# Kernel tuning notes

Measured on AMD Instinct MI355X. Metric: run time of the kernel, lower is better.

The kernel has to match this reference:

```python
import jax, jax.numpy as jnp
import numpy as np

H1, H2, F1, F2 = 16, 16, 8, 1

def gcn_conv(x, src, dst, W, b, n_nodes):
    # PyG GCNConv: add self-loops (done by caller), deg-normalized mean-style aggregation
    h = x @ W  # [N, out]
    deg = jax.ops.segment_sum(jnp.ones_like(dst, dtype=h.dtype), dst, num_segments=n_nodes)
    dinv = jnp.where(deg > 0, deg ** -0.5, 0.0)
    norm = dinv[src] * dinv[dst]  # [E]
    agg = jax.ops.segment_sum(h[src] * norm[:, None], dst, num_segments=n_nodes)
    return agg + b


def setup_inputs() -> dict:
    key = jax.random.key(0)
    ks = jax.random.split(key, 12)
    N, E, G, NG = 320000, 5120000, 1000, 32
    x = jax.random.normal(ks[0], (N, 1), dtype=jnp.float32)
    edge_index = jax.random.randint(ks[1], (2, E), 0, N, dtype=jnp.int64)
    y = jax.random.normal(ks[2], (NG * G,), dtype=jnp.float32)
    gene_idx = jax.random.randint(ks[3], (1, G), 0, N // NG, dtype=jnp.int64)
    s = lambda fi, fo: (2.0 / (fi + fo)) ** 0.5
    return {
        'x': x, 'edge_index': edge_index, 'y': y, 'gene_idx': gene_idx, 'num_graphs': NG,
        'W1': jax.random.normal(ks[4], (1, H1), dtype=jnp.float32) * s(1, H1),
        'b1': jnp.zeros((H1,), dtype=jnp.float32),
        'W2': jax.random.normal(ks[5], (H1, H2), dtype=jnp.float32) * s(H1, H2),
        'b2': jnp.zeros((H2,), dtype=jnp.float32),
        'fc1_W': jax.random.normal(ks[6], (H2, F1), dtype=jnp.float32) * s(H2, F1),
        'fc1_b': jnp.zeros((F1,), dtype=jnp.float32),
        'fc2_W': jax.random.normal(ks[7], (F1, F2), dtype=jnp.float32) * s(F1, F2),
        'fc2_b': jnp.zeros((F2,), dtype=jnp.float32),
    }


def reference(x, edge_index, y, gene_idx, num_graphs, W1, b1, W2, b2, fc1_W, fc1_b, fc2_W, fc2_b):
    N = x.shape[0]
    loops = jnp.arange(N, dtype=edge_index.dtype)
    src = jnp.concatenate([edge_index[0], loops])
    dst = jnp.concatenate([edge_index[1], loops])

    h = jax.nn.relu(gcn_conv(x, src, dst, W1, b1, N))
    # F.dropout(p=0.4) is a no-op for a deterministic reference (identity at eval)
    h = jax.nn.relu(gcn_conv(h, src, dst, W2, b2, N))

    # vectorized form of the python gather loop: idx + i * nodes_per_graph, i = 0..reps-1
    nodes_per_graph = N // num_graphs
    reps = y.shape[0] // gene_idx.shape[1]
    offsets = (jnp.arange(reps, dtype=gene_idx.dtype) * nodes_per_graph)[:, None]
    all_idx = (gene_idx[0][None, :] + offsets).reshape(-1)  # [reps*G]
    t = h[all_idx]  # [reps*G, 16]

    t = jax.nn.relu(t @ fc1_W + fc1_b)
    return t @ fc2_W + fc2_b
```

## Files before the change

kernel.cpp:

```cpp
#include <hip/hip_runtime.h>


#define MAXB 17
#define RS_BITS 10
#define RS (1 << RS_BITS)
#define SRC_BITS 19
#define SRC_MASK ((1u << SRC_BITS) - 1u)
#define SENT 0xFFFFFFFFu
#define CMAX 160
#define NPGW_MAX 2048
#define HB 512
#define BK_BT 512
#define BK_EPT 16
#define BK_TILE (BK_BT * BK_EPT)
#define PAD4(x) (((x) + 3) & ~3)

__device__ __forceinline__ int div_npg(int d, unsigned long long magic) {
    return (int)(((unsigned long long)(unsigned)d * magic) >> 45);
}

__global__ void k_fill_f(float* __restrict__ w, float v, int n) {
    int i = blockIdx.x * blockDim.x + threadIdx.x;
    if (i < n) w[i] = v;
}
__global__ void k_fill_i(int* __restrict__ w, int v, int n) {
    int i = blockIdx.x * blockDim.x + threadIdx.x;
    if (i < n) w[i] = v;
}

__global__ void k_gprep(const float* __restrict__ W1, const float* __restrict__ b1,
                        const int* __restrict__ gene_idx,
                        float* __restrict__ bnd, int* __restrict__ prepI,
                        int* __restrict__ gmap, unsigned* __restrict__ gbit,
                        int* __restrict__ histT, int* __restrict__ histM,
                        int G, int npg, int npgw, int R) {
    int t = threadIdx.x;
    for (int i = t; i < npg; i += 256) gmap[i] = -1;
    for (int i = t; i < npgw; i += 256) gbit[i] = 0;
    for (int i = t; i < R; i += 256) { histT[i] = 0; histM[i] = 0; }
    __syncthreads();
    for (int g = t; g < G; g += 256) {
        int gi = gene_idx[g];
        if ((unsigned)gi < (unsigned)npg) {
            gmap[gi] = g;
            atomicOr(&gbit[gi >> 5], 1u << (gi & 31));
        }
    }
    if (t != 0) return;
    float tt[16]; int type[16]; int pos[16];
    float thr[16]; int nt = 0;
    for (int j = 0; j < 16; j++) {
        float W = W1[j], B = b1[j];
        if (W > 0.f)      { type[j] = 0; tt[j] = -B / W; }
        else if (W < 0.f) { type[j] = 1; tt[j] = -B / W; }
        else              { type[j] = (B > 0.f) ? 2 : 3; tt[j] = 0.f; }
    }
    for (int j = 0; j < 16; j++) {
        if (type[j] > 1) continue;
        float v = tt[j];
        int k = 0; while (k < nt && thr[k] < v) k++;
        if (!(k < nt && thr[k] == v)) {
            for (int m = nt; m > k; m--) thr[m] = thr[m - 1];
            thr[k] = v; nt++;
        }
    }
    int K = nt + 1;
    for (int j = 0; j < 16; j++) {
        if (type[j] <= 1) { int k = 0; while (thr[k] != tt[j]) k++; pos[j] = k; }
        else pos[j] = 0;
    }
    for (int k = 0; k < 16; k++) bnd[k] = (k < nt) ? thr[k] : 3.4e38f;
    prepI[0] = K;
    for (int k = 0; k < K; k++) {
        unsigned m = 0;
        for (int j = 0; j < 16; j++) {
            bool act;
            if (type[j] == 0)      act = (k >= pos[j] + 1);
            else if (type[j] == 1) act = (k <= pos[j]);
            else                   act = (type[j] == 2);
            if (act) m |= (1u << j);
        }
        prepI[1 + k] = (int)m;
    }
}

__global__ void k_cmap_hist(const int* __restrict__ gmap, const unsigned* __restrict__ gbit,
                            const int* __restrict__ dst,
                            int* __restrict__ cm, int* __restrict__ cslot, int* __restrict__ mc,
                            int* __restrict__ histT, int* __restrict__ histM,
                            int N, int R, int npg, int reps, int G, int E, int npgw,
                            unsigned long long magic) {
    __shared__ unsigned bitL[NPGW_MAX];
    for (int i = threadIdx.x; i < npgw; i += 256) bitL[i] = gbit[i];
    if (blockIdx.x < (unsigned)R) {
        __shared__ int cnt;
        if (threadIdx.x == 0) cnt = 0;
        __syncthreads();
        int r = blockIdx.x;
        int b0 = r << RS_BITS;
        for (int i = threadIdx.x; i < RS; i += 256) {
            int v = b0 + i;
            if (v >= N) continue;
            int rep = div_npg(v, magic);
            int gi = v - rep * npg;
            int out = -1;
            if (rep < reps && ((bitL[gi >> 5] >> (gi & 31)) & 1u)) {
                int g = gmap[gi];
                if (g >= 0) {
                    int sl = rep * G + g;
                    int c = atomicAdd(&cnt, 1);
                    if (c < CMAX) { cslot[r * CMAX + c] = sl; out = c; }
                    else out = -(sl + 2);
                }
            }
            cm[v] = out;
        }
        __syncthreads();
        if (threadIdx.x == 0) mc[r] = min(cnt, CMAX);
    } else {
        __shared__ int hT[512], hM[512];
        for (int i = threadIdx.x; i < R; i += 256) { hT[i] = 0; hM[i] = 0; }
        __syncthreads();
        int hb = blockIdx.x - R;
        int stride = HB * 256;
        int E4 = E >> 2;
        const int4* d4p = (const int4*)dst;
        for (int e = hb * 256 + threadIdx.x; e < E4; e += stride) {
            int4 d4 = d4p[e];
            int dd[4] = {d4.x, d4.y, d4.z, d4.w};
#pragma unroll
            for (int k = 0; k < 4; k++) {
                int d = dd[k];
                if ((unsigned)d >= (unsigned)N) continue;
                atomicAdd(&hT[d >> RS_BITS], 1);
                int rep = div_npg(d, magic);
                int gi = d - rep * npg;
                if (rep < reps && ((bitL[gi >> 5] >> (gi & 31)) & 1u))
                    atomicAdd(&hM[d >> RS_BITS], 1);
            }
        }
        for (int e = (E4 << 2) + hb * 256 + threadIdx.x; e < E; e += stride) {
            int d = dst[e];
            if ((unsigned)d >= (unsigned)N) continue;
            atomicAdd(&hT[d >> RS_BITS], 1);
            int rep = div_npg(d, magic);
            int gi = d - rep * npg;
            if (rep < reps && ((bitL[gi >> 5] >> (gi & 31)) & 1u))
                atomicAdd(&hM[d >> RS_BITS], 1);
        }
        __syncthreads();
        for (int i = threadIdx.x; i < R; i += 256) {
            if (hT[i]) atomicAdd(&histT[i], hT[i]);
            if (hM[i]) atomicAdd(&histM[i], hM[i]);
        }
    }
}

__global__ void k_scan(const int* __restrict__ histT, const int* __restrict__ histM,
                       int* __restrict__ baseA, unsigned long long* __restrict__ cur64,
                       unsigned* __restrict__ bucket, int R, int cap) {
    __shared__ int a[512];
    int t = threadIdx.x;
    int m = (t < R) ? histM[t] : 0;
    int tot = (t < R) ? histT[t] : 0;
    int u = tot - m; if (u < 0) u = 0;
    int seg = PAD4(m) + PAD4(u);
    a[t] = seg;
    __syncthreads();
    for (int off = 1; off < 512; off <<= 1) {
        int add = (t >= off) ? a[t - off] : 0;
        __syncthreads();
        a[t] += add;
        __syncthreads();
    }
    if (t < R) {
        int base = a[t] - seg;
        baseA[t] = base;
        int mstart = base, ustart = base + PAD4(m);
        cur64[t] = (unsigned long long)(unsigned)mstart |
                   ((unsigned long long)(unsigned)ustart << 32);
        for (int i = m; i < PAD4(m); i++) { int ix = mstart + i; if (ix < cap) bucket[ix] = SENT; }
        for (int i = u; i < PAD4(u); i++) { int ix = ustart + i; if (ix < cap) bucket[ix] = SENT; }
    }
}

__global__ void __launch_bounds__(BK_BT)
k_bucket(const int* __restrict__ src, const int* __restrict__ dst,
         const unsigned* __restrict__ gbit, unsigned long long* __restrict__ cur64,
         unsigned* __restrict__ bucket, int E, int N, int R, int cap,
         int npg, int reps, int npgw, unsigned long long magic) {
    __shared__ unsigned bitL[NPGW_MAX];
    __shared__ int cntA[512], cntB[512], mb[512], ub[512];
    for (int i = threadIdx.x; i < npgw; i += BK_BT) bitL[i] = gbit[i];
    for (int i = threadIdx.x; i < R; i += BK_BT) { cntA[i] = 0; cntB[i] = 0; }
    __syncthreads();
    int tile0 = blockIdx.x * BK_TILE;
    int rr[BK_EPT]; unsigned val[BK_EPT]; unsigned mbits = 0;
#pragma unroll
    for (int c = 0; c < 4; c++) {
        int e0 = tile0 + c * (BK_BT * 4) + threadIdx.x * 4;
        int dd[4], ss[4];
        if (e0 + 3 < E) {
            int4 d4 = *(const int4*)(dst + e0);
            int4 s4 = *(const int4*)(src + e0);
            dd[0] = d4.x; dd[1] = d4.y; dd[2] = d4.z; dd[3] = d4.w;
            ss[0] = s4.x; ss[1] = s4.y; ss[2] = s4.z; ss[3] = s4.w;
        } else {
#pragma unroll
            for (int k = 0; k < 4; k++) {
                int e = e0 + k;
                dd[k] = (e < E) ? dst[e] : -1;
                ss[k] = (e < E) ? src[e] : -1;
            }
        }
#pragma unroll
        for (int k = 0; k < 4; k++) {
            int idx = c * 4 + k;
            int d = dd[k];
            rr[idx] = -1;
            if ((unsigned)d < (unsigned)N) {
                int rep = div_npg(d, magic);
                int gi = d - rep * npg;
                unsigned m = (rep < reps && ((bitL[gi >> 5] >> (gi & 31)) & 1u)) ? 1u : 0u;
                int s = ss[k];
                rr[idx] = d >> RS_BITS;
                val[idx] = ((unsigned)s < (unsigned)N)
                               ? (((unsigned)(d & (RS - 1)) << SRC_BITS) | (unsigned)s)
                               : SENT;
                mbits |= m << idx;
                atomicAdd(&cntA[d >> RS_BITS], m ? 1 : (1 << 16));
            }
        }
    }
    __syncthreads();
    for (int r = threadIdx.x; r < R; r += BK_BT) {
        int c = cntA[r];
        if (c) {
            unsigned long long add = (unsigned long long)(c & 0xFFFF) |
                                     ((unsigned long long)(unsigned)(c >> 16) << 32);
            unsigned long long old = atomicAdd(&cur64[r], add);
            mb[r] = (int)(old & 0xFFFFFFFFull);
            ub[r] = (int)(old >> 32);
        }
    }
    __syncthreads();
#pragma unroll
    for (int i = 0; i < BK_EPT; i++) {
        int r = rr[i];
        if (r < 0) continue;
        unsigned m = (mbits >> i) & 1u;
        int o = atomicAdd(&cntB[r], m ? 1 : (1 << 16));
        int idx = m ? (mb[r] + (o & 0xFFFF)) : (ub[r] + (o >> 16));
        if ((unsigned)idx < (unsigned)cap) bucket[idx] = val[i];
    }
}


__global__ void __launch_bounds__(1024)
k_degR2(const unsigned* __restrict__ bucket, const int* __restrict__ baseA,
        const int* __restrict__ histT, const int* __restrict__ histM,
        int* __restrict__ pDeg, int cap, int S) {
    __shared__ int degL[RS];
    int r = blockIdx.x / S, q = blockIdx.x % S;
    int m = histM[r];
    int u = histT[r] - m; if (u < 0) u = 0;
    int nb = baseA[r];
    int len = min(PAD4(m) + PAD4(u), cap - nb);
    if (len < 0) len = 0;
    int lo = (int)(((long long)len * q / S) & ~3LL);
    int hi = (q == S - 1) ? len : (int)(((long long)len * (q + 1) / S) & ~3LL);
    for (int i = threadIdx.x; i < RS; i += blockDim.x) degL[i] = 0;
    __syncthreads();
    for (int i = lo + threadIdx.x * 4; i < hi; i += blockDim.x * 4) {
        uint4 e4 = *(const uint4*)(bucket + nb + i);
        if (i + 0 < hi && e4.x != SENT) atomicAdd(&degL[e4.x >> SRC_BITS], 1);
        if (i + 1 < hi && e4.y != SENT) atomicAdd(&degL[e4.y >> SRC_BITS], 1);
        if (i + 2 < hi && e4.z != SENT) atomicAdd(&degL[e4.z >> SRC_BITS], 1);
        if (i + 3 < hi && e4.w != SENT) atomicAdd(&degL[e4.w >> SRC_BITS], 1);
    }
    __syncthreads();
    int* out = pDeg + (size_t)(r * S + q) * RS;
    for (int i = threadIdx.x; i < RS; i += blockDim.x) out[i] = degL[i];
}

__global__ void k_dinvp2(const int* __restrict__ pDeg, const float* __restrict__ x,
                         float* __restrict__ sd, float* __restrict__ p, int N, int S) {
    int v = blockIdx.x * blockDim.x + threadIdx.x;
    if (v >= N) return;
    int r = v >> RS_BITS, l = v & (RS - 1);
    int deg = 0;
    for (int q = 0; q < S; q++) deg += pDeg[(size_t)(r * S + q) * RS + l];
    float di = rsqrtf((float)deg + 1.0f);
    sd[2 * v + 1] = di;
    p[v] = x[v] * di;
}

__global__ void __launch_bounds__(1024)
k_t1R2(const unsigned* __restrict__ bucket, const int* __restrict__ baseA,
       const int* __restrict__ histT, const int* __restrict__ histM,
       const float* __restrict__ p, float* __restrict__ pT1, int cap, int S) {
    __shared__ float accL[RS];
    int r = blockIdx.x / S, q = blockIdx.x % S;
    int m = histM[r];
    int u = histT[r] - m; if (u < 0) u = 0;
    int nb = baseA[r];
    int len = min(PAD4(m) + PAD4(u), cap - nb);
    if (len < 0) len = 0;
    int lo = (int)(((long long)len * q / S) & ~3LL);
    int hi = (q == S - 1) ? len : (int)(((long long)len * (q + 1) / S) & ~3LL);
    for (int i = threadIdx.x; i < RS; i += blockDim.x) accL[i] = 0.f;
    __syncthreads();
    for (int i = lo + threadIdx.x * 4; i < hi; i += blockDim.x * 4) {
        uint4 e4 = *(const uint4*)(bucket + nb + i);
        if (i + 0 < hi && e4.x != SENT) atomicAdd(&accL[e4.x >> SRC_BITS], p[e4.x & SRC_MASK]);
        if (i + 1 < hi && e4.y != SENT) atomicAdd(&accL[e4.y >> SRC_BITS], p[e4.y & SRC_MASK]);
        if (i + 2 < hi && e4.z != SENT) atomicAdd(&accL[e4.z >> SRC_BITS], p[e4.z & SRC_MASK]);
        if (i + 3 < hi && e4.w != SENT) atomicAdd(&accL[e4.w >> SRC_BITS], p[e4.w & SRC_MASK]);
    }
    __syncthreads();
    float* out = pT1 + (size_t)(r * S + q) * RS;
    for (int i = threadIdx.x; i < RS; i += blockDim.x) out[i] = accL[i];
}

__global__ void k_s3(const float* __restrict__ pT1, const float* __restrict__ p,
                     float* __restrict__ sd, float* __restrict__ aggb8, int n8,
                     int N, int S) {
    int v = blockIdx.x * blockDim.x + threadIdx.x;
    if (v < n8) aggb8[v] = 0.f;
    if (v >= N) return;
    int r = v >> RS_BITS, l = v & (RS - 1);
    float t1 = 0.f;
    for (int q = 0; q < S; q++) t1 += pT1[(size_t)(r * S + q) * RS + l];
    sd[2 * v] = sd[2 * v + 1] * (t1 + p[v]);
}

__global__ void k_aggS(const unsigned* __restrict__ bucket, const int* __restrict__ baseA,
                       const int* __restrict__ histM,
                       const float* __restrict__ sd, const int* __restrict__ cm,
                       const int* __restrict__ cslot, const int* __restrict__ mc,
                       const float* __restrict__ bnd, const int* __restrict__ prepI,
                       float* __restrict__ aggb8, int N, int cap) {
    __shared__ float acc[CMAX * 8];
    __shared__ int cmapL[RS];
    __shared__ float sB[3];
    __shared__ int sK;
    if (threadIdx.x == 0) sK = prepI[0];
    if (threadIdx.x < 3) sB[threadIdx.x] = bnd[threadIdx.x];
    __syncthreads();
    int K = sK;
    if (K > 4) return;
    int r = blockIdx.x;
    int b0 = r << RS_BITS;
    for (int i = threadIdx.x; i < RS; i += 256) {
        int v = b0 + i;
        cmapL[i] = (v < N) ? cm[v] : -1;
    }
    for (int i = threadIdx.x; i < CMAX * 8; i += 256) acc[i] = 0.f;
    __syncthreads();
    int nb = baseA[r];
    int mlen = min(histM[r], cap - nb);
    if (mlen < 0) mlen = 0;
    const float2* sd2 = (const float2*)sd;
    for (int i = threadIdx.x * 4; i < mlen; i += 256 * 4) {
        uint4 e4 = *(const uint4*)(bucket + nb + i);
        unsigned ee[4] = {e4.x, e4.y, e4.z, e4.w};
#pragma unroll
        for (int k4 = 0; k4 < 4; k4++) {
            if (i + k4 >= mlen) break;
            unsigned e = ee[k4];
            if (e == SENT) continue;
            int c = cmapL[e >> SRC_BITS];
            if (c == -1) continue;
            float2 v = sd2[e & SRC_MASK];
            int b = 0;
            for (int k = 0; k < K - 1; k++) b += (v.x > sB[k]) ? 1 : 0;
            if (c >= 0) {
                atomicAdd(&acc[c * 8 + 2 * b], v.x * v.y);
                atomicAdd(&acc[c * 8 + 2 * b + 1], v.y);
            } else {
                int sl = -(c + 2);
                atomicAdd(&aggb8[(size_t)sl * 8 + 2 * b], v.x * v.y);
                atomicAdd(&aggb8[(size_t)sl * 8 + 2 * b + 1], v.y);
            }
        }
    }
    __syncthreads();
    int mcR = mc[r];
    for (int idx = threadIdx.x; idx < mcR * 8; idx += 256) {
        int c = idx >> 3, j = idx & 7;
        int sl = cslot[r * CMAX + c];
        if (sl >= 0) aggb8[(size_t)sl * 8 + j] = acc[idx];
    }
}

__global__ void k_fillWide(const int* __restrict__ prepI, float* __restrict__ wide, int n) {
    if (prepI[0] <= 4) return;
    for (int i = blockIdx.x * blockDim.x + threadIdx.x; i < n; i += gridDim.x * blockDim.x)
        wide[i] = 0.f;
}


__global__ void k_mark(const int* __restrict__ gene_idx, int* __restrict__ slot,
                       int G, int M, int npg, int N) {
    int i = blockIdx.x * blockDim.x + threadIdx.x;
    if (i >= M) return;
    int node = gene_idx[i % G] + (i / G) * npg;
    if ((unsigned)node < (unsigned)N) slot[node] = i;
}

__global__ void k_deg(const int* __restrict__ dst, float* __restrict__ deg, int E, int N) {
    int e = blockIdx.x * blockDim.x + threadIdx.x;
    if (e >= E) return;
    int d = dst[e];
    if ((unsigned)d < (unsigned)N) atomicAdd(&deg[d], 1.0f);
}

__global__ void k_dinv_p(const float* __restrict__ x, float* __restrict__ degv,
                         float* __restrict__ p, int N) {
    int v = blockIdx.x * blockDim.x + threadIdx.x;
    if (v < N) {
        float di = rsqrtf(degv[v] + 1.0f);
        degv[v] = di;
        p[v] = x[v] * di;
    }
}

__global__ void k_scatter1(const int* __restrict__ src, const int* __restrict__ dst,
                           const float* __restrict__ p, float* __restrict__ t1, int E, int N) {
    int e = blockIdx.x * blockDim.x + threadIdx.x;
    if (e >= E) return;
    int s = src[e];
    int d = dst[e];
    if ((unsigned)s < (unsigned)N && (unsigned)d < (unsigned)N)
        atomicAdd(&t1[d], p[s]);
}

__global__ void k_s(const float* __restrict__ p, const float* __restrict__ dinv,
                    float* __restrict__ t1, int N) {
    int v = blockIdx.x * blockDim.x + threadIdx.x;
    if (v < N) t1[v] = dinv[v] * (t1[v] + p[v]);
}

__global__ void k_agg_atomic(const int* __restrict__ src, const int* __restrict__ dst,
                             const float* __restrict__ sA, const float* __restrict__ dA,
                             int str, const int* __restrict__ cm, const int* __restrict__ cslot,
                             const float* __restrict__ bnd, const int* __restrict__ prepI,
                             float* __restrict__ wide, int E, int N, int force, int mode) {
    __shared__ float sB[16];
    __shared__ int sK;
    if (threadIdx.x == 0) sK = prepI[0];
    if (threadIdx.x < 16) sB[threadIdx.x] = bnd[threadIdx.x];
    __syncthreads();
    int K = sK;
    if (!force && K <= 4) return;
    int T = K - 1;
    for (int e = blockIdx.x * blockDim.x + threadIdx.x; e < E; e += gridDim.x * blockDim.x) {
        int d = dst[e];
        if ((unsigned)d >= (unsigned)N) continue;
        int c = cm[d];
        int sl;
        if (mode == 0) sl = c;
        else sl = (c >= 0) ? cslot[(d >> RS_BITS) * CMAX + c] : (c <= -2 ? -(c + 2) : -1);
        if (sl < 0) continue;
        int sv = src[e];
        if ((unsigned)sv >= (unsigned)N) continue;
        float sval = sA[(size_t)sv * str];
        float di = dA[(size_t)sv * str];
        int b = 0;
        for (int i = 0; i < T; i++) b += (sval > sB[i]) ? 1 : 0;
        float* row = wide + (size_t)sl * (2 * MAXB) + 2 * b;
        atomicAdd(row, sval * di);
        atomicAdd(row + 1, di);
    }
}

__global__ void k_final(const float* __restrict__ aggb8, const float* __restrict__ wide,
                        const float* __restrict__ sA, const float* __restrict__ dA, int str,
                        const int* __restrict__ gene_idx, const int* __restrict__ cm,
                        const int* __restrict__ cslot, const int* __restrict__ prepI,
                        const float* __restrict__ W1, const float* __restrict__ b1,
                        const float* __restrict__ W2, const float* __restrict__ b2,
                        const float* __restrict__ f1W, const float* __restrict__ f1b,
                        const float* __restrict__ f2W, const float* __restrict__ f2b,
                        float* __restrict__ out, int G, int M, int npg, int N, int mode) {
    __shared__ float sW1[16], sb1[16], sW2[256], sb2[16], sf1[128], sf1b[8], sf2[8], sf2b[1];
    __shared__ int sMask[MAXB], sK;
    for (int i = threadIdx.x; i < 256; i += blockDim.x) sW2[i] = W2[i];
    for (int i = threadIdx.x; i < 128; i += blockDim.x) sf1[i] = f1W[i];
    if (threadIdx.x < 16) { sW1[threadIdx.x] = W1[threadIdx.x]; sb1[threadIdx.x] = b1[threadIdx.x]; sb2[threadIdx.x] = b2[threadIdx.x]; }
    if (threadIdx.x < 8)  { sf1b[threadIdx.x] = f1b[threadIdx.x]; sf2[threadIdx.x] = f2W[threadIdx.x]; }
    if (threadIdx.x == 0) { sf2b[0] = f2b[0]; sK = prepI[0]; }
    if (threadIdx.x < MAXB) sMask[threadIdx.x] = prepI[1 + threadIdx.x];
    __syncthreads();

    int i = blockIdx.x * blockDim.x + threadIdx.x;
    if (i >= M) return;
    int node = gene_idx[i % G] + (i / G) * npg;
    if ((unsigned)node >= (unsigned)N) { out[i] = 0.0f; return; }
    int K = sK;
    int c = cm[node];
    int sl;
    if (mode == 0) sl = c;
    else sl = (c >= 0) ? cslot[(node >> RS_BITS) * CMAX + c] : (c <= -2 ? -(c + 2) : -1);

    float di = dA[(size_t)node * str];
    float sval = sA[(size_t)node * str];

    float bu[MAXB], bw[MAXB];
    if (sl >= 0) {
        const float* row = (mode == 1 && K <= 4) ? (aggb8 + (size_t)sl * 8)
                                                 : (wide + (size_t)sl * (2 * MAXB));
        for (int k = 0; k < K; k++) { bu[k] = row[2 * k]; bw[k] = row[2 * k + 1]; }
    } else {
        for (int k = 0; k < K; k++) { bu[k] = 0.f; bw[k] = 0.f; }
    }

    float a[16];
#pragma unroll
    for (int j = 0; j < 16; j++) {
        float Su = 0.f, Sw = 0.f;
        for (int k = 0; k < K; k++) {
            if ((sMask[k] >> j) & 1) { Su += bu[k]; Sw += bw[k]; }
        }
        float aggj = sW1[j] * Su + sb1[j] * Sw;
        float qself = fmaxf(fmaf(sW1[j], sval, sb1[j]), 0.0f) * di;
        a[j] = di * (aggj + qself);
    }
    float h2[16];
#pragma unroll
    for (int j = 0; j < 16; j++) {
        float acc = sb2[j];
#pragma unroll
        for (int k = 0; k < 16; k++) acc = fmaf(a[k], sW2[k * 16 + j], acc);
        h2[j] = fmaxf(acc, 0.0f);
    }
    float f1[8];
#pragma unroll
    for (int j = 0; j < 8; j++) {
        float acc = sf1b[j];
#pragma unroll
        for (int k = 0; k < 16; k++) acc = fmaf(h2[k], sf1[k * 8 + j], acc);
        f1[j] = fmaxf(acc, 0.0f);
    }
    float o = sf2b[0];
#pragma unroll
    for (int k = 0; k < 8; k++) o = fmaf(f1[k], sf2[k], o);
    out[i] = o;
}

extern "C" void kernel_launch(void* const* d_in, const int* in_sizes, int n_in,
                              void* d_out, int out_size, void* d_ws, size_t ws_size,
                              hipStream_t stream) {
    const float* x        = (const float*)d_in[0];
    const int*   ei       = (const int*)d_in[1];
    const int*   gene_idx = (const int*)d_in[3];
    const float* W1  = (const float*)d_in[5];
    const float* b1  = (const float*)d_in[6];
    const float* W2  = (const float*)d_in[7];
    const float* b2  = (const float*)d_in[8];
    const float* f1W = (const float*)d_in[9];
    const float* f1b = (const float*)d_in[10];
    const float* f2W = (const float*)d_in[11];
    const float* f2b = (const float*)d_in[12];
    float* out = (float*)d_out;

    int N = in_sizes[0];
    int E = in_sizes[1] / 2;
    int M = in_sizes[2];
    int G = in_sizes[3];
    int npg = (int)(((long long)N * (long long)G) / (long long)M);
    int reps = (G > 0) ? M / G : 0;
    int npgw = (npg + 31) / 32;
    unsigned long long magic = (npg >= 1) ? (((1ULL << 45) + npg - 1) / (unsigned)npg) : 1;

    const int* src = ei;
    const int* dst = ei + E;

    int R = (N + RS - 1) >> RS_BITS;
    int cap = E + 8 * R + 8;
    const int tb = 256;

    float* ws = (float*)d_ws;
    size_t off = 0;
    float*    sd     = ws + off;              off += (size_t)2 * N;
    int*      cm     = (int*)(ws + off);      off += (size_t)N;
    float*    p      = ws + off;              off += (size_t)N;
    float*    aggb8  = ws + off;              off += (size_t)8 * M;
    unsigned* bucket = (unsigned*)(ws + off); off += (size_t)cap;
    float*    wide   = (float*)bucket;
    int*      gmap   = (int*)(ws + off);      off += (size_t)npg;
    unsigned* gbit   = (unsigned*)(ws + off); off += (size_t)npgw;
    int*      cslot  = (int*)(ws + off);      off += (size_t)R * CMAX;
    int*      mc     = (int*)(ws + off);      off += (size_t)R;
    int*      histT  = (int*)(ws + off);      off += (size_t)R;
    int*      histM  = (int*)(ws + off);      off += (size_t)R;
    int*      baseA  = (int*)(ws + off);      off += (size_t)R;
    off = (off + 1) & ~(size_t)1;
    unsigned long long* cur64 = (unsigned long long*)(ws + off); off += (size_t)2 * R;
    float*    bnd    = ws + off;              off += 16;
    int*      prepI  = (int*)(ws + off);      off += 20;
    size_t base_need = off;

    int S = 4;
    while (S > 1 && (base_need + (size_t)R * S * RS) * 4 > ws_size) S >>= 1;
    float* partial = ws + base_need;
    int*   partialI = (int*)partial;
    size_t need = (base_need + (size_t)R * S * RS) * 4;

    bool use_new = (need <= ws_size) && (N < (1 << SRC_BITS)) && (R <= 512) &&
                   (npg >= 1) && (npg <= NPGW_MAX * 32) && (reps >= 1) &&
                   ((size_t)cap * 4 >= (size_t)2 * MAXB * M * 4);

    if (use_new) {
        int BTr = (S == 1) ? 1024 : 256;
        k_gprep<<<1, 256, 0, stream>>>(W1, b1, gene_idx, bnd, prepI, gmap, gbit,
                                       histT, histM, G, npg, npgw, R);
        k_cmap_hist<<<R + HB, 256, 0, stream>>>(gmap, gbit, dst, cm, cslot, mc,
                                                histT, histM, N, R, npg, reps, G, E,
                                                npgw, magic);
        k_scan<<<1, 512, 0, stream>>>(histT, histM, baseA, cur64, bucket, R, cap);
        int ntiles = (E + BK_TILE - 1) / BK_TILE;
        k_bucket<<<ntiles, BK_BT, 0, stream>>>(src, dst, gbit, cur64, bucket,
                                               E, N, R, cap, npg, reps, npgw, magic);
        k_degR2<<<R * S, BTr, 0, stream>>>(bucket, baseA, histT, histM, partialI, cap, S);
        k_dinvp2<<<(N + tb - 1) / tb, tb, 0, stream>>>(partialI, x, sd, p, N, S);
        k_t1R2<<<R * S, BTr, 0, stream>>>(bucket, baseA, histT, histM, p, partial, cap, S);
        int n8 = 8 * M;
        int s3grid = ((N > n8 ? N : n8) + tb - 1) / tb;
        k_s3<<<s3grid, tb, 0, stream>>>(partial, p, sd, aggb8, n8, N, S);
        k_aggS<<<R, tb, 0, stream>>>(bucket, baseA, histM, sd, cm, cslot, mc,
                                     bnd, prepI, aggb8, N, cap);
        int wn = 2 * MAXB * M;
        k_fillWide<<<512, tb, 0, stream>>>(prepI, wide, wn);
        k_agg_atomic<<<512, tb, 0, stream>>>(src, dst, sd, sd + 1, 2, cm, cslot, bnd,
                                             prepI, wide, E, N, 0, 1);
        k_final<<<(M + tb - 1) / tb, tb, 0, stream>>>(aggb8, wide, sd, sd + 1, 2, gene_idx,
                                                      cm, cslot, prepI, W1, b1, W2, b2,
                                                      f1W, f1b, f2W, f2b, out, G, M, npg, N,
                                                      1);
    } else {
        float* deg   = ws;
        float* t1o   = ws + (size_t)N;
        float* pO    = ws + 2 * (size_t)N;
        int*   slotO = (int*)(ws + 3 * (size_t)N);
        float* wideO = ws + 4 * (size_t)N;
        float* bndO  = wideO + (size_t)2 * MAXB * M;
        int*   prepO = (int*)(bndO + 16);
        int*   scr   = prepO + 20;

        k_fill_f<<<(2 * N + tb - 1) / tb, tb, 0, stream>>>(deg, 0.0f, 2 * N);
        k_fill_i<<<(N + tb - 1) / tb, tb, 0, stream>>>(slotO, -1, N);
        k_fill_f<<<(2 * MAXB * M + tb - 1) / tb, tb, 0, stream>>>(wideO, 0.0f, 2 * MAXB * M);
        k_gprep<<<1, 256, 0, stream>>>(W1, b1, gene_idx, bndO, prepO,
                                       scr, (unsigned*)(scr + 1), scr + 2, scr + 3,
                                       0, 1, 1, 0);
        k_mark<<<(M + tb - 1) / tb, tb, 0, stream>>>(gene_idx, slotO, G, M, npg, N);
        k_deg<<<(E + tb - 1) / tb, tb, 0, stream>>>(dst, deg, E, N);
        k_dinv_p<<<(N + tb - 1) / tb, tb, 0, stream>>>(x, deg, pO, N);
        k_scatter1<<<(E + tb - 1) / tb, tb, 0, stream>>>(src, dst, pO, t1o, E, N);
        k_s<<<(N + tb - 1) / tb, tb, 0, stream>>>(pO, deg, t1o, N);
        k_agg_atomic<<<2048, tb, 0, stream>>>(src, dst, t1o, deg, 1, slotO, (int*)0, bndO,
                                              prepO, wideO, E, N, 1, 0);
        k_final<<<(M + tb - 1) / tb, tb, 0, stream>>>((float*)0, wideO, t1o, deg, 1, gene_idx,
                                                      slotO, (int*)0, prepO, W1, b1, W2, b2,
                                                      f1W, f1b, f2W, f2b, out, G, M, npg, N,
                                                      0);
    }
}
```

Before: 253.6 us.

## Stage bucket scatter through shared-memory local sort for coalesced global writes

In k_bucket, each block now builds an exclusive prefix scan of its per-bucket counts (split by marked and unmarked class). It places every edge into a shared-memory staging array ordered by bucket, then writes the staging array to global memory contiguously using per-class address deltas. This replaces scattered per-edge global stores with mostly contiguous runs, aiming to improve write coalescing. In exchange it adds a block-wide scan, extra barriers and about 48KB of shared memory, which may lower occupancy. RMAX and NPGW_MAX shrink to fit that memory, which narrows the inputs the fast path accepts.

```diff
diff --git a/kernel.cpp b/kernel.cpp
--- a/kernel.cpp
+++ b/kernel.cpp
@@ -8,7 +8,8 @@
 #define SRC_MASK ((1u << SRC_BITS) - 1u)
 #define SENT 0xFFFFFFFFu
 #define CMAX 160
-#define NPGW_MAX 2048
+#define RMAX 320
+#define NPGW_MAX 512
 #define HB 512
 #define BK_BT 512
 #define BK_EPT 16
@@ -118,7 +119,7 @@
         __syncthreads();
         if (threadIdx.x == 0) mc[r] = min(cnt, CMAX);
     } else {
-        __shared__ int hT[512], hM[512];
+        __shared__ int hT[RMAX], hM[RMAX];
         for (int i = threadIdx.x; i < R; i += 256) { hT[i] = 0; hM[i] = 0; }
         __syncthreads();
         int hb = blockIdx.x - R;
@@ -190,10 +191,18 @@
          unsigned* __restrict__ bucket, int E, int N, int R, int cap,
          int npg, int reps, int npgw, unsigned long long magic) {
     __shared__ unsigned bitL[NPGW_MAX];
-    __shared__ int cntA[512], cntB[512], mb[512], ub[512];
+    __shared__ int cntA[RMAX];
+    __shared__ int cnt2[RMAX];
+    __shared__ int eb[2 * RMAX];
+    __shared__ int dl[2 * RMAX];
+    __shared__ unsigned sortL[BK_TILE];
+    __shared__ unsigned short clsL[BK_TILE];
+    __shared__ int totalS;
+
     for (int i = threadIdx.x; i < npgw; i += BK_BT) bitL[i] = gbit[i];
-    for (int i = threadIdx.x; i < R; i += BK_BT) { cntA[i] = 0; cntB[i] = 0; }
-    __syncthreads();
+    for (int i = threadIdx.x; i < R; i += BK_BT) { cntA[i] = 0; cnt2[i] = 0; }
+    __syncthreads();
+
     int tile0 = blockIdx.x * BK_TILE;
     int rr[BK_EPT]; unsigned val[BK_EPT]; unsigned mbits = 0;
 #pragma unroll
@@ -233,14 +242,39 @@
         }
     }
     __syncthreads();
+    int n2 = 2 * R;
+    for (int i = threadIdx.x; i < n2; i += BK_BT)
+        eb[i] = (i < R) ? (cntA[i] & 0xFFFF) : (cntA[i - R] >> 16);
+    __syncthreads();
+    for (int off = 1; off < n2; off <<= 1) {
+        int i0 = threadIdx.x, i1 = threadIdx.x + BK_BT;
+        int t0 = 0, t1 = 0;
+        if (i0 < n2 && i0 >= off) t0 = eb[i0 - off];
+        if (i1 < n2 && i1 >= off) t1 = eb[i1 - off];
+        __syncthreads();
+        if (i0 < n2) eb[i0] += t0;
+        if (i1 < n2) eb[i1] += t1;
+        __syncthreads();
+    }
+    if (threadIdx.x == 0) totalS = eb[n2 - 1];
+    {
+        int i0 = threadIdx.x, i1 = threadIdx.x + BK_BT;
+        int c0 = 0, c1 = 0;
+        if (i0 < n2) c0 = (i0 < R) ? (cntA[i0] & 0xFFFF) : (cntA[i0 - R] >> 16);
+        if (i1 < n2) c1 = (i1 < R) ? (cntA[i1] & 0xFFFF) : (cntA[i1 - R] >> 16);
+        __syncthreads();
+        if (i0 < n2) eb[i0] -= c0;
+        if (i1 < n2) eb[i1] -= c1;
+    }
+    __syncthreads();
     for (int r = threadIdx.x; r < R; r += BK_BT) {
         int c = cntA[r];
         if (c) {
             unsigned long long add = (unsigned long long)(c & 0xFFFF) |
                                      ((unsigned long long)(unsigned)(c >> 16) << 32);
             unsigned long long old = atomicAdd(&cur64[r], add);
-            mb[r] = (int)(old & 0xFFFFFFFFull);
-            ub[r] = (int)(old >> 32);
+            dl[r]     = (int)(old & 0xFFFFFFFFull) - eb[r];
+            dl[R + r] = (int)(old >> 32)           - eb[R + r];
         }
     }
     __syncthreads();
@@ -249,9 +283,19 @@
         int r = rr[i];
         if (r < 0) continue;
         unsigned m = (mbits >> i) & 1u;
-        int o = atomicAdd(&cntB[r], m ? 1 : (1 << 16));
-        int idx = m ? (mb[r] + (o & 0xFFFF)) : (ub[r] + (o >> 16));
-        if ((unsigned)idx < (unsigned)cap) bucket[idx] = val[i];
+        int o = atomicAdd(&cnt2[r], m ? 1 : (1 << 16));
+        int cidx = m ? r : (R + r);
+        int loc = m ? (o & 0xFFFF) : (o >> 16);
+        int pos = eb[cidx] + loc;
+        sortL[pos] = val[i];
+        clsL[pos] = (unsigned short)cidx;
+    }
+    __syncthreads();
+    int total = totalS;
+    for (int i = threadIdx.x; i < total; i += BK_BT) {
+        int cidx = clsL[i];
+        int addr = dl[cidx] + i;
+        if ((unsigned)addr < (unsigned)cap) bucket[addr] = sortL[i];
     }
 }
 
@@ -607,7 +651,7 @@
     int*   partialI = (int*)partial;
     size_t need = (base_need + (size_t)R * S * RS) * 4;
 
-    bool use_new = (need <= ws_size) && (N < (1 << SRC_BITS)) && (R <= 512) &&
+    bool use_new = (need <= ws_size) && (N < (1 << SRC_BITS)) && (R <= RMAX) &&
                    (npg >= 1) && (npg <= NPGW_MAX * 32) && (reps >= 1) &&
                    ((size_t)cap * 4 >= (size_t)2 * MAXB * M * 4);
 
```

New measurement: 250.0 us. No clear change (-1.4%).
